# Optimization experiments

Hardware: AMD Instinct MI355X
Metric: run time of the kernel (lower is better)

The kernel has to match this reference:

```python
import jax, jax.numpy as jnp
import numpy as np

N, E, F, R, S = 20000, 320000, 64, 8, 10
AVG_NEIGH = 16.0


def setup_inputs() -> dict:
    key = jax.random.key(0)
    ks = jax.random.split(key, 16)
    inp = {
        "vectors": jax.random.normal(ks[0], (E, 3), jnp.float32),
        "node_feats": jax.random.normal(ks[1], (N, F, 4), jnp.float32),  # [N, F, 1(0e)+3(1o)]
        "node_specie": jax.random.randint(ks[2], (N,), 0, S),
        "radial_embedding": jax.random.normal(ks[3], (E, R), jnp.float32),
        "senders": jax.random.randint(ks[4], (E,), 0, N),
        "receivers": jax.random.randint(ks[5], (E,), 0, N),
        # residual FullyConnectedTensorProduct(feats, one-hot species 0e) == species-dep. linear per l
        "W_res_s": jax.random.normal(ks[6], (S, F, F), jnp.float32),
        "W_res_v": jax.random.normal(ks[7], (S, F, F), jnp.float32),
        # interaction block: input linear per l
        "W_in_s": jax.random.normal(ks[8], (F, F), jnp.float32),
        "W_in_v": jax.random.normal(ks[9], (F, F), jnp.float32),
        # radial MLP -> 5 CG tensor-product path weights per channel
        "mlp_w1": jax.random.normal(ks[10], (R, 64), jnp.float32),
        "mlp_w2": jax.random.normal(ks[11], (64, 5 * F), jnp.float32) / 8.0,
        # interaction block: output linear per l
        "W_out_s": jax.random.normal(ks[12], (F, F), jnp.float32),
        "W_out_v": jax.random.normal(ks[13], (F, F), jnp.float32),
        # symmetric product basis (correlation 3), species-dependent term weights
        "W_prod_s": jax.random.normal(ks[14], (S, 5, F), jnp.float32) * 0.3,
        "W_prod_v": jax.random.normal(ks[15], (S, 4, F), jnp.float32) * 0.3,
    }
    k2 = jax.random.split(jax.random.key(1), 3)
    inp["W_lin_s"] = jax.random.normal(k2[0], (F, F), jnp.float32)
    inp["W_lin_v"] = jax.random.normal(k2[1], (F, F), jnp.float32)
    inp["W_read"] = jax.random.normal(k2[2], (F, 1), jnp.float32)
    return inp


def _forward(vectors, node_feats, node_specie, radial_embedding, senders, receivers,
             W_res_s, W_res_v, W_in_s, W_in_v, mlp_w1, mlp_w2, W_out_s, W_out_v,
             W_prod_s, W_prod_v, W_lin_s, W_lin_v, W_read):
    inv_sf = 1.0 / jnp.sqrt(jnp.float32(F))
    s = node_feats[..., 0]          # [N,F]   0e channels
    v = node_feats[..., 1:]         # [N,F,3] 1o channels

    # --- residual connection: FCTP(feats, one-hot species 0e attrs) -> species-gated linear per l
    res_s = jnp.einsum('nf,ngf->ng', s, W_res_s[node_specie]) * inv_sf
    res_v = jnp.einsum('nfc,ngf->ngc', v, W_res_v[node_specie]) * inv_sf

    # --- InteractionBlock ---
    h_s = (s @ W_in_s) * inv_sf
    h_v = jnp.einsum('nfc,fg->ngc', v, W_in_v) * inv_sf

    # spherical harmonics up to max_ell=1: Y0 = 1, Y1 = unit edge vector
    r = jnp.sqrt(jnp.sum(vectors * vectors, -1) + 1e-12)
    Y1 = vectors / r[:, None]                                # [E,3]

    # radial MLP produces per-edge weights for the 5 CG paths:
    # (0e x Y0 -> 0e), (1o . Y1 -> 0e), (0e x Y1 -> 1o), (1o x Y0 -> 1o), (1o x Y1 -> 1o, cross)
    w = (jax.nn.silu(radial_embedding @ mlp_w1) @ mlp_w2).reshape(-1, 5, F)  # [E,5,F]

    ss = h_s[senders]                                        # [E,F]
    sv = h_v[senders]                                        # [E,F,3]
    dot = jnp.einsum('efc,ec->ef', sv, Y1)                   # [E,F]
    m_s = w[:, 0] * ss + w[:, 1] * dot                       # [E,F]
    m_v = (w[:, 2] * ss)[:, :, None] * Y1[:, None, :] \
        + w[:, 3][:, :, None] * sv \
        + w[:, 4][:, :, None] * jnp.cross(sv, Y1[:, None, :])  # [E,F,3]

    agg_s = jnp.zeros_like(h_s).at[receivers].add(m_s) / AVG_NEIGH
    agg_v = jnp.zeros_like(h_v).at[receivers].add(m_v) / AVG_NEIGH
    a_s = (agg_s @ W_out_s) * inv_sf
    a_v = jnp.einsum('nfc,fg->ngc', agg_v, W_out_v) * inv_sf

    # --- EquivariantProductBasisBlock: correlation-3 symmetric contraction, species-dependent ---
    vv = jnp.sum(a_v * a_v, -1)                              # [N,F] invariant |v|^2
    Wp = W_prod_s[node_specie]                               # [N,5,F]
    p_s = (Wp[:, 0] * a_s + Wp[:, 1] * a_s ** 2 + Wp[:, 2] * a_s ** 3
           + Wp[:, 3] * vv + Wp[:, 4] * a_s * vv)
    Wv = W_prod_v[node_specie]                               # [N,4,F]
    p_v = (Wv[:, 0] + Wv[:, 1] * a_s + Wv[:, 2] * a_s ** 2 + Wv[:, 3] * vv)[:, :, None] * a_v

    f_s = (p_s @ W_lin_s) * inv_sf + res_s
    f_v = jnp.einsum('nfc,fg->ngc', p_v, W_lin_v) * inv_sf + res_v

    # --- LinearReadoutBlock (output_irreps = 0e), 1 head ---
    node_out = ((f_s @ W_read) * inv_sf)[:, None, :]         # [N, heads=1, 1]
    new_feats = jnp.concatenate([f_s[..., None], f_v], axis=-1)  # [N,F,4]
    return node_out, new_feats


def reference(vectors, node_feats, node_specie, radial_embedding, senders, receivers,
              W_res_s, W_res_v, W_in_s, W_in_v, mlp_w1, mlp_w2, W_out_s, W_out_v,
              W_prod_s, W_prod_v, W_lin_s, W_lin_v, W_read):
    return _forward(vectors, node_feats, node_specie, radial_embedding, senders, receivers,
                    W_res_s, W_res_v, W_in_s, W_in_v, mlp_w1, mlp_w2, W_out_s, W_out_v,
                    W_prod_s, W_prod_v, W_lin_s, W_lin_v, W_read)
```

## Files before the change

### kernel.cpp

```cpp
#include <hip/hip_runtime.h>
#include <math.h>

#define NN 20000
#define NE 320000
#define NF (NN*64)
#define TB 16

__global__ __launch_bounds__(256) void k_transpose_res(
    const float* __restrict__ Ws, const float* __restrict__ Wv,
    float* __restrict__ Wst, float* __restrict__ Wvt)
{
  int i = blockIdx.x*256 + threadIdx.x;
  int spec = i >> 12;
  int g = (i >> 6) & 63;
  int f = i & 63;
  Wst[spec*4096 + f*64 + g] = Ws[i];
  Wvt[spec*4096 + f*64 + g] = Wv[i];
}

__global__ __launch_bounds__(256) void k_hist(const int* __restrict__ receivers,
                                              int* __restrict__ count)
{
  int e = blockIdx.x*256 + threadIdx.x;
  atomicAdd(&count[receivers[e]], 1);
}

__global__ __launch_bounds__(256) void k_scan(const int* __restrict__ count,
                                              int* __restrict__ offset)
{
  __shared__ int part[256];
  int t = threadIdx.x;
  const int PER = 79;
  int s = 0;
  for(int i=0;i<PER;++i){ int idx = t*PER+i; if(idx < NN) s += count[idx]; }
  part[t] = s;
  __syncthreads();
  for(int off=1; off<256; off<<=1){
    int v = (t>=off) ? part[t-off] : 0;
    __syncthreads();
    part[t] += v;
    __syncthreads();
  }
  int run = t ? part[t-1] : 0;
  for(int i=0;i<PER;++i){
    int idx = t*PER+i;
    if(idx < NN){ offset[idx] = run; run += count[idx]; }
  }
  if(t==255) offset[NN] = run;
}

__global__ __launch_bounds__(256) void k_scatter(
    const int* __restrict__ receivers, const int* __restrict__ offset,
    int* __restrict__ count, int* __restrict__ order)
{
  int e = blockIdx.x*256 + threadIdx.x;
  int r = receivers[e];
  int old = atomicSub(&count[r], 1);
  order[offset[r] + old - 1] = e;
}

__global__ __launch_bounds__(256) void k_node_pre(
    const float* __restrict__ node_feats, const float* __restrict__ W_in_s,
    const float* __restrict__ W_in_v, float* __restrict__ h)
{
  __shared__ float sh[16][4][64];
  int wave = threadIdx.x >> 6, lane = threadIdx.x & 63;
  int nb = blockIdx.x*16 + wave*4;
  #pragma unroll
  for(int k=0;k<4;++k){
    int nd = wave*4 + k;
    float4 nf = *(const float4*)(node_feats + (size_t)((nb+k)*64 + lane)*4);
    sh[nd][0][lane]=nf.x; sh[nd][1][lane]=nf.y; sh[nd][2][lane]=nf.z; sh[nd][3][lane]=nf.w;
  }
  __syncthreads();
  float as[4]={0,0,0,0}, a0[4]={0,0,0,0}, a1[4]={0,0,0,0}, a2[4]={0,0,0,0};
  for(int f=0; f<64; ++f){
    float ws = W_in_s[f*64+lane], wv = W_in_v[f*64+lane];
    #pragma unroll
    for(int k=0;k<4;++k){
      int nd = wave*4 + k;
      as[k] = fmaf(sh[nd][0][f], ws, as[k]);
      a0[k] = fmaf(sh[nd][1][f], wv, a0[k]);
      a1[k] = fmaf(sh[nd][2][f], wv, a1[k]);
      a2[k] = fmaf(sh[nd][3][f], wv, a2[k]);
    }
  }
  #pragma unroll
  for(int k=0;k<4;++k){
    size_t o = (size_t)(nb+k)*256 + lane;
    h[o]     = as[k]*0.125f;
    h[o+64]  = a0[k]*0.125f;
    h[o+128] = a1[k]*0.125f;
    h[o+192] = a2[k]*0.125f;
  }
}

__global__ __launch_bounds__(256) void k_edge(
    const float* __restrict__ vectors, const float* __restrict__ radial,
    const int* __restrict__ senders, const int* __restrict__ receivers,
    const float* __restrict__ mlp_w1, const float* __restrict__ mlp_w2,
    const float* __restrict__ h, const int* __restrict__ order,
    float* __restrict__ agg)
{
  __shared__ int   eidS[4][TB];
  __shared__ int   sndS[4][TB];
  __shared__ int   rcvS[4][TB];
  __shared__ float vecS[4][3*TB];
  __shared__ float rad[4][8*TB];
  __shared__ float hid[4][TB][64];
  int wave = threadIdx.x >> 6, lane = threadIdx.x & 63;
  int e0 = (blockIdx.x*4 + wave)*TB;

  if(lane < TB){
    int e = order[e0 + lane];
    eidS[wave][lane] = e;
    sndS[wave][lane] = senders[e];
    rcvS[wave][lane] = receivers[e];
  }
  float wl[8];
  #pragma unroll
  for(int r=0;r<8;++r) wl[r] = mlp_w1[r*64+lane];
  __syncthreads();
  if(lane < 3*TB) vecS[wave][lane] = vectors[(size_t)eidS[wave][lane/3]*3 + lane%3];
  rad[wave][lane]    = radial[(size_t)eidS[wave][lane>>3]*8     + (lane&7)];
  rad[wave][64+lane] = radial[(size_t)eidS[wave][8+(lane>>3)]*8 + (lane&7)];
  __syncthreads();
  #pragma unroll
  for(int t=0;t<TB;++t){
    float acc = 0.f;
    #pragma unroll
    for(int r=0;r<8;++r) acc = fmaf(rad[wave][t*8+r], wl[r], acc);
    hid[wave][t][lane] = acc / (1.f + __expf(-acc));
  }
  __syncthreads();
  float w[5][TB];
  #pragma unroll
  for(int j=0;j<5;++j)
    #pragma unroll
    for(int t=0;t<TB;++t) w[j][t] = 0.f;
  for(int hh=0; hh<64; hh+=2){
    float b0[5], b1[5];
    #pragma unroll
    for(int j=0;j<5;++j){
      b0[j] = mlp_w2[hh*320     + j*64 + lane];
      b1[j] = mlp_w2[(hh+1)*320 + j*64 + lane];
    }
    #pragma unroll
    for(int t=0;t<TB;++t){
      float2 hb = *(const float2*)&hid[wave][t][hh];
      #pragma unroll
      for(int j=0;j<5;++j) w[j][t] = fmaf(hb.x, b0[j], fmaf(hb.y, b1[j], w[j][t]));
    }
  }
  float as_=0.f, av0=0.f, av1=0.f, av2=0.f;
  int cur = rcvS[wave][0];
  #pragma unroll
  for(int t=0;t<TB;++t){
    int rcv = rcvS[wave][t];
    if(rcv != cur){
      size_t ro = (size_t)cur*256 + lane;
      atomicAdd(&agg[ro],     as_);
      atomicAdd(&agg[ro+64],  av0);
      atomicAdd(&agg[ro+128], av1);
      atomicAdd(&agg[ro+192], av2);
      as_=0.f; av0=0.f; av1=0.f; av2=0.f;
      cur = rcv;
    }
    int snd = sndS[wave][t];
    float vx=vecS[wave][t*3], vy=vecS[wave][t*3+1], vz=vecS[wave][t*3+2];
    float rinv = rsqrtf(vx*vx + vy*vy + vz*vz + 1e-12f);
    float y0=vx*rinv, y1=vy*rinv, y2=vz*rinv;
    size_t so = (size_t)snd*256 + lane;
    float ss  = h[so];
    float sv0 = h[so+64], sv1 = h[so+128], sv2 = h[so+192];
    float dot = sv0*y0 + sv1*y1 + sv2*y2;
    as_ += w[0][t]*ss + w[1][t]*dot;
    float w2s = w[2][t]*ss, w3t = w[3][t], w4t = w[4][t];
    av0 += w2s*y0 + w3t*sv0 + w4t*(sv1*y2 - sv2*y1);
    av1 += w2s*y1 + w3t*sv1 + w4t*(sv2*y0 - sv0*y2);
    av2 += w2s*y2 + w3t*sv2 + w4t*(sv0*y1 - sv1*y0);
  }
  size_t ro = (size_t)cur*256 + lane;
  atomicAdd(&agg[ro],     as_);
  atomicAdd(&agg[ro+64],  av0);
  atomicAdd(&agg[ro+128], av1);
  atomicAdd(&agg[ro+192], av2);
}

__global__ __launch_bounds__(256) void k_node_post(
  const float* __restrict__ node_feats, const int* __restrict__ specie,
  const float* __restrict__ agg,
  const float* __restrict__ Wrst, const float* __restrict__ Wrvt,
  const float* __restrict__ W_out_s, const float* __restrict__ W_out_v,
  const float* __restrict__ W_prod_s, const float* __restrict__ W_prod_v,
  const float* __restrict__ W_lin_s, const float* __restrict__ W_lin_v,
  const float* __restrict__ W_read, float* __restrict__ out_node,
  float* __restrict__ out_feats)
{
  __shared__ float shA[16][4][64];
  __shared__ float shS[16][4][64];
  int wave = threadIdx.x >> 6, lane = threadIdx.x & 63;
  int nb = blockIdx.x*16 + wave*4;
  #pragma unroll
  for(int k=0;k<4;++k){
    int nd = wave*4 + k;
    size_t o = (size_t)(nb+k)*256 + lane;
    shA[nd][0][lane] = agg[o]     * (1.f/16.f);
    shA[nd][1][lane] = agg[o+64]  * (1.f/16.f);
    shA[nd][2][lane] = agg[o+128] * (1.f/16.f);
    shA[nd][3][lane] = agg[o+192] * (1.f/16.f);
    float4 nf = *(const float4*)(node_feats + (size_t)((nb+k)*64 + lane)*4);
    shS[nd][0][lane]=nf.x; shS[nd][1][lane]=nf.y; shS[nd][2][lane]=nf.z; shS[nd][3][lane]=nf.w;
  }
  int spec[4];
  #pragma unroll
  for(int k=0;k<4;++k) spec[k] = specie[nb+k];
  __syncthreads();
  float a_s[4]={0,0,0,0}, a0[4]={0,0,0,0}, a1[4]={0,0,0,0}, a2[4]={0,0,0,0};
  float r_s[4]={0,0,0,0}, r0[4]={0,0,0,0}, r1[4]={0,0,0,0}, r2[4]={0,0,0,0};
  for(int f=0; f<64; ++f){
    float wos = W_out_s[f*64+lane], wov = W_out_v[f*64+lane];
    #pragma unroll
    for(int k=0;k<4;++k){
      int nd = wave*4 + k;
      a_s[k] = fmaf(shA[nd][0][f], wos, a_s[k]);
      a0[k]  = fmaf(shA[nd][1][f], wov, a0[k]);
      a1[k]  = fmaf(shA[nd][2][f], wov, a1[k]);
      a2[k]  = fmaf(shA[nd][3][f], wov, a2[k]);
    }
    #pragma unroll
    for(int k=0;k<4;++k){
      int nd = wave*4 + k;
      float wrs = Wrst[spec[k]*4096 + f*64 + lane];
      float wrv = Wrvt[spec[k]*4096 + f*64 + lane];
      r_s[k] = fmaf(shS[nd][0][f], wrs, r_s[k]);
      r0[k]  = fmaf(shS[nd][1][f], wrv, r0[k]);
      r1[k]  = fmaf(shS[nd][2][f], wrv, r1[k]);
      r2[k]  = fmaf(shS[nd][3][f], wrv, r2[k]);
    }
  }
  __syncthreads();
  #pragma unroll
  for(int k=0;k<4;++k){
    int nd = wave*4 + k;
    float A_s = a_s[k]*0.125f, A0 = a0[k]*0.125f, A1 = a1[k]*0.125f, A2 = a2[k]*0.125f;
    float vv = A0*A0 + A1*A1 + A2*A2;
    float as2 = A_s*A_s;
    const float* Wp = W_prod_s + spec[k]*320;
    float p_s = Wp[lane]*A_s + Wp[64+lane]*as2 + Wp[128+lane]*as2*A_s
              + Wp[192+lane]*vv + Wp[256+lane]*A_s*vv;
    const float* Wq = W_prod_v + spec[k]*256;
    float coef = Wq[lane] + Wq[64+lane]*A_s + Wq[128+lane]*as2 + Wq[192+lane]*vv;
    shS[nd][0][lane] = p_s;
    shS[nd][1][lane] = coef*A0;
    shS[nd][2][lane] = coef*A1;
    shS[nd][3][lane] = coef*A2;
  }
  __syncthreads();
  float lfs[4]={0,0,0,0}, lf0[4]={0,0,0,0}, lf1[4]={0,0,0,0}, lf2[4]={0,0,0,0};
  for(int f=0; f<64; ++f){
    float wls = W_lin_s[f*64+lane], wlv = W_lin_v[f*64+lane];
    #pragma unroll
    for(int k=0;k<4;++k){
      int nd = wave*4 + k;
      lfs[k] = fmaf(shS[nd][0][f], wls, lfs[k]);
      lf0[k] = fmaf(shS[nd][1][f], wlv, lf0[k]);
      lf1[k] = fmaf(shS[nd][2][f], wlv, lf1[k]);
      lf2[k] = fmaf(shS[nd][3][f], wlv, lf2[k]);
    }
  }
  float wr = W_read[lane];
  #pragma unroll
  for(int k=0;k<4;++k){
    int n = nb + k;
    float FS = lfs[k]*0.125f + r_s[k]*0.125f;
    float F0 = lf0[k]*0.125f + r0[k]*0.125f;
    float F1 = lf1[k]*0.125f + r1[k]*0.125f;
    float F2 = lf2[k]*0.125f + r2[k]*0.125f;
    float x = FS * wr;
    #pragma unroll
    for(int off=32; off; off>>=1) x += __shfl_down(x, off);
    if(lane==0) out_node[n] = x*0.125f;
    float4 o4; o4.x=FS; o4.y=F0; o4.z=F1; o4.w=F2;
    *(float4*)(out_feats + (size_t)(n*64+lane)*4) = o4;
  }
}

extern "C" void kernel_launch(void* const* d_in, const int* in_sizes, int n_in,
                              void* d_out, int out_size, void* d_ws, size_t ws_size,
                              hipStream_t stream) {
  const float* vectors    = (const float*)d_in[0];
  const float* node_feats = (const float*)d_in[1];
  const int*   node_specie= (const int*)  d_in[2];
  const float* radial     = (const float*)d_in[3];
  const int*   senders    = (const int*)  d_in[4];
  const int*   receivers  = (const int*)  d_in[5];
  const float* W_res_s    = (const float*)d_in[6];
  const float* W_res_v    = (const float*)d_in[7];
  const float* W_in_s     = (const float*)d_in[8];
  const float* W_in_v     = (const float*)d_in[9];
  const float* mlp_w1     = (const float*)d_in[10];
  const float* mlp_w2     = (const float*)d_in[11];
  const float* W_out_s    = (const float*)d_in[12];
  const float* W_out_v    = (const float*)d_in[13];
  const float* W_prod_s   = (const float*)d_in[14];
  const float* W_prod_v   = (const float*)d_in[15];
  const float* W_lin_s    = (const float*)d_in[16];
  const float* W_lin_v    = (const float*)d_in[17];
  const float* W_read     = (const float*)d_in[18];

  float* ws   = (float*)d_ws;
  float* h    = ws;
  float* agg  = ws + 4*(size_t)NF;
  float* Wrst = ws + 8*(size_t)NF;
  float* Wrvt = Wrst + 40960;
  int*   order  = (int*)(Wrvt + 40960);
  int*   offset = order + NE;
  int*   count  = offset + NN + 1;

  hipMemsetAsync(agg,   0, (size_t)4*NF*sizeof(float), stream);
  hipMemsetAsync(count, 0, (size_t)NN*sizeof(int), stream);
  k_transpose_res<<<160, 256, 0, stream>>>(W_res_s, W_res_v, Wrst, Wrvt);
  k_hist   <<<NE/256, 256, 0, stream>>>(receivers, count);
  k_scan   <<<1,      256, 0, stream>>>(count, offset);
  k_scatter<<<NE/256, 256, 0, stream>>>(receivers, offset, count, order);
  k_node_pre<<<NN/16, 256, 0, stream>>>(node_feats, W_in_s, W_in_v, h);
  k_edge<<<NE/(4*TB), 256, 0, stream>>>(vectors, radial, senders, receivers,
                                        mlp_w1, mlp_w2, h, order, agg);
  k_node_post<<<NN/16, 256, 0, stream>>>(node_feats, node_specie, agg,
                                         Wrst, Wrvt, W_out_s, W_out_v,
                                         W_prod_s, W_prod_v, W_lin_s, W_lin_v,
                                         W_read, (float*)d_out, (float*)d_out + NN);
}
```

Measured before the change: 509.3 us.

## Pre-sort edge data by receiver and interleave node features as float4

The histogram pass now records each edge's rank, which removes the atomicSub in the scatter. The scatter writes senders, receivers, normalized direction vectors and radial embeddings into receiver-sorted contiguous arrays, so the edge kernel no longer does indirect gathers through an order array and no longer needs its __syncthreads. The h and agg buffers switch to a per-channel interleaved [N,64,4] layout, so each sender gather and each node_post load is a single float4. Sender rows are also prefetched four edges ahead. The cost is an extra pass writing about 13 words per edge of sorted data, plus atomics on adjacent addresses.

```diff
diff --git a/kernel.cpp b/kernel.cpp
--- a/kernel.cpp
+++ b/kernel.cpp
@@ -18,11 +18,12 @@
   Wvt[spec*4096 + f*64 + g] = Wv[i];
 }
 
-__global__ __launch_bounds__(256) void k_hist(const int* __restrict__ receivers,
-                                              int* __restrict__ count)
+__global__ __launch_bounds__(256) void k_hist_rank(const int* __restrict__ receivers,
+                                                   int* __restrict__ count,
+                                                   int* __restrict__ rank)
 {
   int e = blockIdx.x*256 + threadIdx.x;
-  atomicAdd(&count[receivers[e]], 1);
+  rank[e] = atomicAdd(&count[receivers[e]], 1);
 }
 
 __global__ __launch_bounds__(256) void k_scan(const int* __restrict__ count,
@@ -50,13 +51,25 @@
 }
 
 __global__ __launch_bounds__(256) void k_scatter(
-    const int* __restrict__ receivers, const int* __restrict__ offset,
-    int* __restrict__ count, int* __restrict__ order)
+    const int* __restrict__ senders, const int* __restrict__ receivers,
+    const float* __restrict__ vectors, const float* __restrict__ radial,
+    const int* __restrict__ offset, const int* __restrict__ rank,
+    int* __restrict__ srt_snd, int* __restrict__ srt_rcv,
+    float* __restrict__ srt_y, float* __restrict__ srt_rad)
 {
   int e = blockIdx.x*256 + threadIdx.x;
   int r = receivers[e];
-  int old = atomicSub(&count[r], 1);
-  order[offset[r] + old - 1] = e;
+  int slot = offset[r] + rank[e];
+  srt_snd[slot] = senders[e];
+  srt_rcv[slot] = r;
+  float vx = vectors[e*3], vy = vectors[e*3+1], vz = vectors[e*3+2];
+  float rinv = rsqrtf(vx*vx + vy*vy + vz*vz + 1e-12f);
+  float4 y4; y4.x = vx*rinv; y4.y = vy*rinv; y4.z = vz*rinv; y4.w = 0.f;
+  *(float4*)(srt_y + (size_t)slot*4) = y4;
+  float4 ra = *(const float4*)(radial + (size_t)e*8);
+  float4 rb = *(const float4*)(radial + (size_t)e*8 + 4);
+  *(float4*)(srt_rad + (size_t)slot*8)     = ra;
+  *(float4*)(srt_rad + (size_t)slot*8 + 4) = rb;
 }
 
 __global__ __launch_bounds__(256) void k_node_pre(
@@ -87,44 +100,37 @@
   }
   #pragma unroll
   for(int k=0;k<4;++k){
-    size_t o = (size_t)(nb+k)*256 + lane;
-    h[o]     = as[k]*0.125f;
-    h[o+64]  = a0[k]*0.125f;
-    h[o+128] = a1[k]*0.125f;
-    h[o+192] = a2[k]*0.125f;
+    float4 o4; o4.x = as[k]*0.125f; o4.y = a0[k]*0.125f;
+    o4.z = a1[k]*0.125f; o4.w = a2[k]*0.125f;
+    *(float4*)(h + (size_t)((nb+k)*64 + lane)*4) = o4;
   }
 }
 
 __global__ __launch_bounds__(256) void k_edge(
-    const float* __restrict__ vectors, const float* __restrict__ radial,
-    const int* __restrict__ senders, const int* __restrict__ receivers,
+    const float* __restrict__ srt_y, const float* __restrict__ srt_rad,
+    const int* __restrict__ srt_snd, const int* __restrict__ srt_rcv,
     const float* __restrict__ mlp_w1, const float* __restrict__ mlp_w2,
-    const float* __restrict__ h, const int* __restrict__ order,
-    float* __restrict__ agg)
-{
-  __shared__ int   eidS[4][TB];
+    const float* __restrict__ h, float* __restrict__ agg)
+{
   __shared__ int   sndS[4][TB];
   __shared__ int   rcvS[4][TB];
-  __shared__ float vecS[4][3*TB];
+  __shared__ float yS[4][4*TB];
   __shared__ float rad[4][8*TB];
   __shared__ float hid[4][TB][64];
   int wave = threadIdx.x >> 6, lane = threadIdx.x & 63;
   int e0 = (blockIdx.x*4 + wave)*TB;
 
   if(lane < TB){
-    int e = order[e0 + lane];
-    eidS[wave][lane] = e;
-    sndS[wave][lane] = senders[e];
-    rcvS[wave][lane] = receivers[e];
-  }
+    sndS[wave][lane] = srt_snd[e0 + lane];
+    rcvS[wave][lane] = srt_rcv[e0 + lane];
+  }
+  yS[wave][lane]     = srt_y[(size_t)e0*4 + lane];
+  rad[wave][lane]    = srt_rad[(size_t)e0*8 + lane];
+  rad[wave][64+lane] = srt_rad[(size_t)e0*8 + 64 + lane];
   float wl[8];
   #pragma unroll
   for(int r=0;r<8;++r) wl[r] = mlp_w1[r*64+lane];
-  __syncthreads();
-  if(lane < 3*TB) vecS[wave][lane] = vectors[(size_t)eidS[wave][lane/3]*3 + lane%3];
-  rad[wave][lane]    = radial[(size_t)eidS[wave][lane>>3]*8     + (lane&7)];
-  rad[wave][64+lane] = radial[(size_t)eidS[wave][8+(lane>>3)]*8 + (lane&7)];
-  __syncthreads();
+
   #pragma unroll
   for(int t=0;t<TB;++t){
     float acc = 0.f;
@@ -132,7 +138,7 @@
     for(int r=0;r<8;++r) acc = fmaf(rad[wave][t*8+r], wl[r], acc);
     hid[wave][t][lane] = acc / (1.f + __expf(-acc));
   }
-  __syncthreads();
+
   float w[5][TB];
   #pragma unroll
   for(int j=0;j<5;++j)
@@ -152,27 +158,31 @@
       for(int j=0;j<5;++j) w[j][t] = fmaf(hb.x, b0[j], fmaf(hb.y, b1[j], w[j][t]));
     }
   }
+
+  float4 hv[4];
+  #pragma unroll
+  for(int p=0;p<4;++p)
+    hv[p] = *(const float4*)(h + (size_t)(sndS[wave][p]*64 + lane)*4);
+
   float as_=0.f, av0=0.f, av1=0.f, av2=0.f;
   int cur = rcvS[wave][0];
   #pragma unroll
   for(int t=0;t<TB;++t){
+    float4 hc = hv[t&3];
+    if(t+4 < TB)
+      hv[t&3] = *(const float4*)(h + (size_t)(sndS[wave][t+4]*64 + lane)*4);
     int rcv = rcvS[wave][t];
     if(rcv != cur){
-      size_t ro = (size_t)cur*256 + lane;
-      atomicAdd(&agg[ro],     as_);
-      atomicAdd(&agg[ro+64],  av0);
-      atomicAdd(&agg[ro+128], av1);
-      atomicAdd(&agg[ro+192], av2);
+      size_t ro = (size_t)(cur*64 + lane)*4;
+      atomicAdd(&agg[ro],   as_);
+      atomicAdd(&agg[ro+1], av0);
+      atomicAdd(&agg[ro+2], av1);
+      atomicAdd(&agg[ro+3], av2);
       as_=0.f; av0=0.f; av1=0.f; av2=0.f;
       cur = rcv;
     }
-    int snd = sndS[wave][t];
-    float vx=vecS[wave][t*3], vy=vecS[wave][t*3+1], vz=vecS[wave][t*3+2];
-    float rinv = rsqrtf(vx*vx + vy*vy + vz*vz + 1e-12f);
-    float y0=vx*rinv, y1=vy*rinv, y2=vz*rinv;
-    size_t so = (size_t)snd*256 + lane;
-    float ss  = h[so];
-    float sv0 = h[so+64], sv1 = h[so+128], sv2 = h[so+192];
+    float y0=yS[wave][t*4], y1=yS[wave][t*4+1], y2=yS[wave][t*4+2];
+    float ss=hc.x, sv0=hc.y, sv1=hc.z, sv2=hc.w;
     float dot = sv0*y0 + sv1*y1 + sv2*y2;
     as_ += w[0][t]*ss + w[1][t]*dot;
     float w2s = w[2][t]*ss, w3t = w[3][t], w4t = w[4][t];
@@ -180,11 +190,11 @@
     av1 += w2s*y1 + w3t*sv1 + w4t*(sv2*y0 - sv0*y2);
     av2 += w2s*y2 + w3t*sv2 + w4t*(sv0*y1 - sv1*y0);
   }
-  size_t ro = (size_t)cur*256 + lane;
-  atomicAdd(&agg[ro],     as_);
-  atomicAdd(&agg[ro+64],  av0);
-  atomicAdd(&agg[ro+128], av1);
-  atomicAdd(&agg[ro+192], av2);
+  size_t ro = (size_t)(cur*64 + lane)*4;
+  atomicAdd(&agg[ro],   as_);
+  atomicAdd(&agg[ro+1], av0);
+  atomicAdd(&agg[ro+2], av1);
+  atomicAdd(&agg[ro+3], av2);
 }
 
 __global__ __launch_bounds__(256) void k_node_post(
@@ -204,11 +214,11 @@
   #pragma unroll
   for(int k=0;k<4;++k){
     int nd = wave*4 + k;
-    size_t o = (size_t)(nb+k)*256 + lane;
-    shA[nd][0][lane] = agg[o]     * (1.f/16.f);
-    shA[nd][1][lane] = agg[o+64]  * (1.f/16.f);
-    shA[nd][2][lane] = agg[o+128] * (1.f/16.f);
-    shA[nd][3][lane] = agg[o+192] * (1.f/16.f);
+    float4 ag = *(const float4*)(agg + (size_t)((nb+k)*64 + lane)*4);
+    shA[nd][0][lane] = ag.x * (1.f/16.f);
+    shA[nd][1][lane] = ag.y * (1.f/16.f);
+    shA[nd][2][lane] = ag.z * (1.f/16.f);
+    shA[nd][3][lane] = ag.w * (1.f/16.f);
     float4 nf = *(const float4*)(node_feats + (size_t)((nb+k)*64 + lane)*4);
     shS[nd][0][lane]=nf.x; shS[nd][1][lane]=nf.y; shS[nd][2][lane]=nf.z; shS[nd][3][lane]=nf.w;
   }
@@ -314,19 +324,24 @@
   float* agg  = ws + 4*(size_t)NF;
   float* Wrst = ws + 8*(size_t)NF;
   float* Wrvt = Wrst + 40960;
-  int*   order  = (int*)(Wrvt + 40960);
-  int*   offset = order + NE;
-  int*   count  = offset + NN + 1;
+  float* srt_rad = Wrvt + 40960;
+  float* srt_y   = srt_rad + 8*(size_t)NE;
+  int*   srt_snd = (int*)(srt_y + 4*(size_t)NE);
+  int*   srt_rcv = srt_snd + NE;
+  int*   rank    = srt_rcv + NE;
+  int*   offset  = rank + NE;
+  int*   count   = offset + NN + 1;
 
   hipMemsetAsync(agg,   0, (size_t)4*NF*sizeof(float), stream);
   hipMemsetAsync(count, 0, (size_t)NN*sizeof(int), stream);
   k_transpose_res<<<160, 256, 0, stream>>>(W_res_s, W_res_v, Wrst, Wrvt);
-  k_hist   <<<NE/256, 256, 0, stream>>>(receivers, count);
-  k_scan   <<<1,      256, 0, stream>>>(count, offset);
-  k_scatter<<<NE/256, 256, 0, stream>>>(receivers, offset, count, order);
+  k_hist_rank<<<NE/256, 256, 0, stream>>>(receivers, count, rank);
+  k_scan     <<<1,      256, 0, stream>>>(count, offset);
+  k_scatter  <<<NE/256, 256, 0, stream>>>(senders, receivers, vectors, radial,
+                                          offset, rank, srt_snd, srt_rcv, srt_y, srt_rad);
   k_node_pre<<<NN/16, 256, 0, stream>>>(node_feats, W_in_s, W_in_v, h);
-  k_edge<<<NE/(4*TB), 256, 0, stream>>>(vectors, radial, senders, receivers,
-                                        mlp_w1, mlp_w2, h, order, agg);
+  k_edge<<<NE/(4*TB), 256, 0, stream>>>(srt_y, srt_rad, srt_snd, srt_rcv,
+                                        mlp_w1, mlp_w2, h, agg);
   k_node_post<<<NN/16, 256, 0, stream>>>(node_feats, node_specie, agg,
                                          Wrst, Wrvt, W_out_s, W_out_v,
                                          W_prod_s, W_prod_v, W_lin_s, W_lin_v,
```

Result: slower. 536.7 us (+5.4%).
